# Performance work log

Hardware: AMD Instinct MI355X
Metric: run time of the kernel (lower is better)

The kernel has to match this reference:

```python
import jax, jax.numpy as jnp
import numpy as np

B, IN, O, F, FH = 512, 2000, 64, 8, 32
D = 64 + FH * O  # 2112


def setup_inputs() -> dict:
    key = jax.random.key(0)
    ks = jax.random.split(key, 17)
    rn = lambda k, s: jax.random.normal(k, s, dtype=jnp.float32) * 0.05
    return dict(
        x=rn(ks[0], (B, IN)),
        fc_in_W=rn(ks[1], (1024, IN)), fc_in_b=rn(ks[2], (1024,)),
        fc1_W=rn(ks[3], (128, 1024)), fc1_b=rn(ks[4], (128,)),
        out1_W=rn(ks[5], (O, 64, 128)), out1_b=rn(ks[6], (O, 64)),
        coef_nn_W=rn(ks[7], (F, FH, 1)), coef_nn_b=rn(ks[8], (F, FH)),
        coef_att_W=rn(ks[9], (F, FH, FH)),
        out_att_W=rn(ks[10], (O, FH, FH)),
        nodes_trans_W=rn(ks[11], (O, O)),
        trans_gcn_W=rn(ks[12], (D, D)),
        outmap_W=rn(ks[13], (1, D)), outmap_b=rn(ks[14], (1,)),
        prelu_a=jnp.float32(0.25),
        coef_m=rn(ks[15], (O, O, F)),
    )


def reference(x, fc_in_W, fc_in_b, fc1_W, fc1_b, out1_W, out1_b,
              coef_nn_W, coef_nn_b, coef_att_W, out_att_W,
              nodes_trans_W, trans_gcn_W, outmap_W, outmap_b, prelu_a, coef_m):
    elu = jax.nn.elu
    # trunk MLP
    h = jax.nn.relu(x @ fc_in_W.T + fc_in_b)          # [B,1024]
    h = jax.nn.relu(h @ fc1_W.T + fc1_b)              # [B,128]
    # per-output-node heads (vectorized over the output_dim loop)
    hiddens = jax.nn.relu(jnp.einsum('bk,odk->bod', h, out1_W) + out1_b)  # [B,O,64]
    # per-feature coef embedding: Linear(1,FH) on each coef_m[:,:,i] slice
    cf = elu(coef_m[..., None] * coef_nn_W[:, :, 0] + coef_nn_b)          # [O,O,F,FH]
    # sum over concatenated feature axis (F*FH) of exp(elu(.))
    s = jnp.exp(elu(cf)).sum(axis=(2, 3))[:, :, None, None]               # [O,O,1,1]
    lin = jnp.einsum('xyfh,fgh->xyfg', cf, coef_att_W)                    # per-feature attention linear
    p = elu(jnp.exp(elu(cf)) * lin / s)
    cfs = elu(p.sum(axis=2) / F)                                          # [O,O,FH]
    # node-level attention (vectorized over the output_dim loop)
    coef_sum = jnp.exp(elu(cfs)).sum(axis=1)                              # [O,FH]
    p2 = jnp.exp(elu(cfs)) / coef_sum[:, None, :]                         # [O,O,FH]
    lin2 = jnp.einsum('oih,igh->oig', cfs, out_att_W)
    att = (p2 * lin2).reshape(O, O * FH)                                  # concat over i (i-major)
    hc = jnp.concatenate(
        [hiddens, jnp.broadcast_to(att[None], (x.shape[0], O, O * FH))], axis=2)  # [B,O,D]
    nt = jnp.einsum('bpd,op->bod', hc, nodes_trans_W)                     # node mixing Linear(O,O)
    trans = jax.nn.sigmoid(jnp.einsum('bod,ed->boe', nt, trans_gcn_W))    # [B,O,D]
    z = (trans @ outmap_W.T + outmap_b).squeeze(-1)                       # [B,O]
    return jnp.where(z >= 0, z, prelu_a * z)                              # PReLU
```

## Files before the change

### kernel.cpp

```cpp
#include <hip/hip_runtime.h>
#include <math.h>

typedef __attribute__((ext_vector_type(8))) short bf16x8;
typedef __attribute__((ext_vector_type(4))) float f32x4;

static __device__ __forceinline__ float fast_elu(float x) {
    return x > 0.0f ? x : __expf(x) - 1.0f;
}

static __device__ __forceinline__ unsigned short f2bf(float f) {
    unsigned int u = __float_as_uint(f);
    unsigned int r = (u + 0x7FFFu + ((u >> 16) & 1u)) >> 16;
    return (unsigned short)r;
}

#define CV0 1048576
#define CV1 3145728
#define CV2 3276800
#define CV3 3280896
#define CV4 3805184
#define CV5 8265728
#define CONV_BLOCKS 32288

static __device__ __forceinline__ void conv_phase(
    int bx,
    const float* __restrict__ x, const float* __restrict__ fcinW,
    const float* __restrict__ fc1W, const float* __restrict__ ntW,
    const float* __restrict__ out1W, const float* __restrict__ tgw,
    unsigned short* __restrict__ xb, unsigned short* __restrict__ fcinWb,
    unsigned short* __restrict__ fc1Wb, unsigned short* __restrict__ Wb,
    unsigned short* __restrict__ out1WbT,
    unsigned short* __restrict__ Gb, unsigned short* __restrict__ G2b)
{
    int idx = bx * 256 + threadIdx.x;
    if (idx < CV0) {
        int r = idx >> 11, k = idx & 2047;
        xb[idx] = (k < 2000) ? f2bf(x[(size_t)r * 2000 + k]) : (unsigned short)0;
    } else if (idx < CV1) {
        int i = idx - CV0;
        int r = i >> 11, k = i & 2047;
        fcinWb[i] = (k < 2000) ? f2bf(fcinW[(size_t)r * 2000 + k]) : (unsigned short)0;
    } else if (idx < CV2) {
        int i = idx - CV1;
        fc1Wb[i] = f2bf(fc1W[i]);
    } else if (idx < CV3) {
        int i = idx - CV2;
        Wb[i] = f2bf(ntW[i]);
    } else if (idx < CV4) {
        int i = idx - CV3;
        int n = i >> 7, k = i & 127, d = n >> 6, p = n & 63;
        out1WbT[i] = f2bf(out1W[(size_t)((p << 6) | d) * 128 + k]);
    } else if (idx < CV5) {
        int i = idx - CV4;
        int e = i / 2112, k = i - e * 2112;
        unsigned short v = f2bf(tgw[(size_t)e * 2112 + k]);
        if (k < 64) Gb[e * 64 + k] = v;
        else        G2b[(size_t)e * 2048 + (k - 64)] = v;
    }
}

static __device__ __forceinline__ void coef_phase(
    int bx, float* __restrict__ smemf,
    const float* __restrict__ coef_m, const float* __restrict__ cW,
    const float* __restrict__ cB, const float* __restrict__ attW,
    float* __restrict__ cfs)
{
    float* cf_s = smemf;
    float* part = smemf + 1024;
    const int t = threadIdx.x;
    const int wv = t >> 6, lane = t & 63;
    const int xy = bx * 4 + wv;
    float ls = 0.0f;
    #pragma unroll
    for (int i = 0; i < 4; ++i) {
        int idx = i * 64 + lane;
        int f = idx >> 5;
        float v = fast_elu(coef_m[xy * 8 + f] * cW[idx] + cB[idx]);
        cf_s[wv * 256 + idx] = v;
        ls += __expf(fast_elu(v));
    }
    #pragma unroll
    for (int m = 1; m < 64; m <<= 1) ls += __shfl_xor(ls, m, 64);
    __syncthreads();
    const float rs = __builtin_amdgcn_rcpf(ls);
    const int g = lane & 31, fg = lane >> 5;
    float acc = 0.0f;
    for (int f = fg * 4; f < fg * 4 + 4; ++f) {
        float lin = 0.0f;
        #pragma unroll
        for (int h = 0; h < 32; h += 4) {
            float4 Lv = *reinterpret_cast<const float4*>(&cf_s[wv * 256 + f * 32 + h]);
            float4 Wv = *reinterpret_cast<const float4*>(&attW[f * 1024 + g * 32 + h]);
            lin += Lv.x * Wv.x + Lv.y * Wv.y + Lv.z * Wv.z + Lv.w * Wv.w;
        }
        float e = __expf(fast_elu(cf_s[wv * 256 + f * 32 + g]));
        acc += fast_elu(e * lin * rs);
    }
    part[wv * 64 + lane] = acc;
    __syncthreads();
    if (lane < 32) {
        float tot = part[wv * 64 + lane] + part[wv * 64 + lane + 32];
        cfs[xy * 32 + lane] = fast_elu(tot * 0.125f);
    }
}

static __device__ __forceinline__ void att_phase(
    int o, int ic, float* __restrict__ smemf,
    const float* __restrict__ cfs, const float* __restrict__ oattW,
    float* __restrict__ att)
{
    float* L    = smemf;
    float* red  = smemf + 2048;
    float* csum = smemf + 2304;
    const int t = threadIdx.x;
    #pragma unroll
    for (int j = 0; j < 8; ++j) L[t + 256 * j] = cfs[o * 2048 + t + 256 * j];
    __syncthreads();
    {
        int h = t & 31, ig = t >> 5;
        float ps = 0.0f;
        for (int i = ig * 8; i < ig * 8 + 8; ++i) ps += __expf(fast_elu(L[i * 32 + h]));
        red[t] = ps;
        __syncthreads();
        if (t < 32) {
            float cs = 0.0f;
            #pragma unroll
            for (int j = 0; j < 8; ++j) cs += red[j * 32 + t];
            csum[t] = cs;
        }
        __syncthreads();
    }
    int idx = ic * 256 + t;
    int i = idx >> 5, g = idx & 31;
    float lin2 = 0.0f;
    #pragma unroll
    for (int h = 0; h < 32; h += 4) {
        float4 Lv = *reinterpret_cast<const float4*>(&L[i * 32 + h]);
        float4 Wv = *reinterpret_cast<const float4*>(&oattW[i * 1024 + g * 32 + h]);
        lin2 += Lv.x * Wv.x + Lv.y * Wv.y + Lv.z * Wv.z + Lv.w * Wv.w;
    }
    float p2 = __expf(fast_elu(L[idx])) * __builtin_amdgcn_rcpf(csum[g]);
    att[o * 2048 + idx] = p2 * lin2;
}

static __device__ __forceinline__ void natt_phase(
    int bx, float* __restrict__ smemf,
    const float* __restrict__ ntW, const float* __restrict__ att,
    unsigned short* __restrict__ nattb)
{
    float* ntW_s = smemf;
    float* att_s = smemf + 64 * 65;
    const int t = threadIdx.x;
    const int d0 = bx * 16;
    #pragma unroll
    for (int j = 0; j < 16; ++j) {
        int idx = t + 256 * j;
        ntW_s[(idx >> 6) * 65 + (idx & 63)] = ntW[idx];
    }
    #pragma unroll
    for (int j = 0; j < 4; ++j) {
        int idx = t + 256 * j;
        int p = idx >> 4, dd = idx & 15;
        att_s[p * 17 + dd] = att[p * 2048 + d0 + dd];
    }
    __syncthreads();
    const int dd = t & 15, ob = (t >> 4) * 4;
    float acc[4] = {0.0f, 0.0f, 0.0f, 0.0f};
    for (int p = 0; p < 64; ++p) {
        float av = att_s[p * 17 + dd];
        #pragma unroll
        for (int i = 0; i < 4; ++i) acc[i] += ntW_s[(ob + i) * 65 + p] * av;
    }
    #pragma unroll
    for (int i = 0; i < 4; ++i)
        nattb[(ob + i) * 2048 + d0 + dd] = f2bf(acc[i]);
}

static __device__ __forceinline__ void gemm_core(
    const unsigned short* __restrict__ A, int lda,
    const unsigned short* __restrict__ B, int ldb,
    float* __restrict__ C, unsigned short* __restrict__ Cb,
    int ldc, long strideCz, const float* __restrict__ bias,
    int mode, int kchunk, int bn, int bm, int bz,
    unsigned short* __restrict__ As, unsigned short* __restrict__ Bs)
{
    const int t = threadIdx.x;
    const int w = t >> 6, lane = t & 63, l16 = lane & 15, quad = lane >> 4;
    const int n0 = bn * 64, m0 = bm * 64;
    const int kb0 = bz * kchunk;
    const int r = t >> 2, koff = (t & 3) * 8;
    if (mode == 0) C += (size_t)bz * strideCz;

    const size_t arow = (size_t)(m0 + r) * lda + koff;
    const size_t brow = (size_t)(n0 + r) * ldb + koff;
    bf16x8 av = *reinterpret_cast<const bf16x8*>(&A[arow + kb0]);
    bf16x8 bv = *reinterpret_cast<const bf16x8*>(&B[brow + kb0]);

    f32x4 acc[4] = {};
    for (int kb = kb0; kb < kb0 + kchunk; kb += 32) {
        __syncthreads();
        *reinterpret_cast<bf16x8*>(&As[r * 40 + koff]) = av;
        *reinterpret_cast<bf16x8*>(&Bs[r * 40 + koff]) = bv;
        if (kb + 32 < kb0 + kchunk) {
            av = *reinterpret_cast<const bf16x8*>(&A[arow + kb + 32]);
            bv = *reinterpret_cast<const bf16x8*>(&B[brow + kb + 32]);
        }
        __syncthreads();
        bf16x8 af = *reinterpret_cast<const bf16x8*>(&As[(w * 16 + l16) * 40 + quad * 8]);
        #pragma unroll
        for (int nt = 0; nt < 4; ++nt) {
            bf16x8 bf = *reinterpret_cast<const bf16x8*>(&Bs[(nt * 16 + l16) * 40 + quad * 8]);
            acc[nt] = __builtin_amdgcn_mfma_f32_16x16x32_bf16(af, bf, acc[nt], 0, 0, 0);
        }
    }
    #pragma unroll
    for (int nt = 0; nt < 4; ++nt)
        #pragma unroll
        for (int i = 0; i < 4; ++i) {
            int m = m0 + w * 16 + quad * 4 + i;
            int n = n0 + nt * 16 + l16;
            if (mode == 0) {
                C[(size_t)m * ldc + n] = acc[nt][i];
            } else {
                int bidx = (((n & 63) << 6) | (n >> 6));
                float v = acc[nt][i] + bias[bidx];
                v = fmaxf(v, 0.0f);
                Cb[(size_t)m * ldc + n] = f2bf(v);
            }
        }
}

static __device__ __forceinline__ void gemm_fa_core(
    const float* __restrict__ Ap, int lda, long apstride, int nparts,
    const float* __restrict__ abias,
    const unsigned short* __restrict__ B, int ldb,
    float* __restrict__ C, unsigned short* __restrict__ Cb,
    int ldc, long strideCz, const float* __restrict__ bias,
    int mode, int kchunk, int bn, int bm, int bz,
    unsigned short* __restrict__ As, unsigned short* __restrict__ Bs)
{
    const int t = threadIdx.x;
    const int w = t >> 6, lane = t & 63, l16 = lane & 15, quad = lane >> 4;
    const int n0 = bn * 64, m0 = bm * 64;
    const int kb0 = bz * kchunk;
    const int r = t >> 2, koff = (t & 3) * 8;
    if (mode == 0) C += (size_t)bz * strideCz;

    f32x4 acc[4] = {};
    for (int kb = kb0; kb < kb0 + kchunk; kb += 32) {
        float a8[8];
        {
            const float* base = &Ap[(size_t)(m0 + r) * lda + kb + koff];
            float4 s0 = *reinterpret_cast<const float4*>(base);
            float4 s1 = *reinterpret_cast<const float4*>(base + 4);
            for (int j = 1; j < nparts; ++j) {
                const float* pj = base + (size_t)j * apstride;
                float4 p0 = *reinterpret_cast<const float4*>(pj);
                float4 p1 = *reinterpret_cast<const float4*>(pj + 4);
                s0.x += p0.x; s0.y += p0.y; s0.z += p0.z; s0.w += p0.w;
                s1.x += p1.x; s1.y += p1.y; s1.z += p1.z; s1.w += p1.w;
            }
            float4 b0 = *reinterpret_cast<const float4*>(&abias[kb + koff]);
            float4 b1 = *reinterpret_cast<const float4*>(&abias[kb + koff + 4]);
            a8[0] = fmaxf(s0.x + b0.x, 0.0f); a8[1] = fmaxf(s0.y + b0.y, 0.0f);
            a8[2] = fmaxf(s0.z + b0.z, 0.0f); a8[3] = fmaxf(s0.w + b0.w, 0.0f);
            a8[4] = fmaxf(s1.x + b1.x, 0.0f); a8[5] = fmaxf(s1.y + b1.y, 0.0f);
            a8[6] = fmaxf(s1.z + b1.z, 0.0f); a8[7] = fmaxf(s1.w + b1.w, 0.0f);
        }
        bf16x8 bv = *reinterpret_cast<const bf16x8*>(&B[(size_t)(n0 + r) * ldb + kb + koff]);
        __syncthreads();
        ushort4 lo, hi;
        lo.x = f2bf(a8[0]); lo.y = f2bf(a8[1]); lo.z = f2bf(a8[2]); lo.w = f2bf(a8[3]);
        hi.x = f2bf(a8[4]); hi.y = f2bf(a8[5]); hi.z = f2bf(a8[6]); hi.w = f2bf(a8[7]);
        *reinterpret_cast<ushort4*>(&As[r * 40 + koff]) = lo;
        *reinterpret_cast<ushort4*>(&As[r * 40 + koff + 4]) = hi;
        *reinterpret_cast<bf16x8*>(&Bs[r * 40 + koff]) = bv;
        __syncthreads();
        bf16x8 af = *reinterpret_cast<const bf16x8*>(&As[(w * 16 + l16) * 40 + quad * 8]);
        #pragma unroll
        for (int nt = 0; nt < 4; ++nt) {
            bf16x8 bf = *reinterpret_cast<const bf16x8*>(&Bs[(nt * 16 + l16) * 40 + quad * 8]);
            acc[nt] = __builtin_amdgcn_mfma_f32_16x16x32_bf16(af, bf, acc[nt], 0, 0, 0);
        }
    }
    #pragma unroll
    for (int nt = 0; nt < 4; ++nt)
        #pragma unroll
        for (int i = 0; i < 4; ++i) {
            int m = m0 + w * 16 + quad * 4 + i;
            int n = n0 + nt * 16 + l16;
            if (mode == 0) {
                C[(size_t)m * ldc + n] = acc[nt][i];
            } else {
                int bidx = (((n & 63) << 6) | (n >> 6));
                float v = acc[nt][i] + bias[bidx];
                v = fmaxf(v, 0.0f);
                Cb[(size_t)m * ldc + n] = f2bf(v);
            }
        }
}

static __device__ __forceinline__ void nt1f_phase(
    int b, unsigned short* __restrict__ smemu,
    const unsigned short* __restrict__ hbT, const unsigned short* __restrict__ Wb,
    unsigned short* __restrict__ nt1b)
{
    unsigned short* HtT   = smemu;
    unsigned short* nt1_s = smemu + 64 * 72;
    const int t = threadIdx.x;
    const int w = t >> 6, lane = t & 63, l16 = lane & 15, quad = lane >> 4;

    const unsigned short* src = hbT + (size_t)b * 4096;
    #pragma unroll
    for (int j = 0; j < 2; ++j) {
        int c = t + j * 256;
        *reinterpret_cast<bf16x8*>(&HtT[(c >> 3) * 72 + (c & 7) * 8]) =
            *reinterpret_cast<const bf16x8*>(&src[c * 8]);
    }
    __syncthreads();

    bf16x8 aW[2];
    #pragma unroll
    for (int h = 0; h < 2; ++h)
        aW[h] = *reinterpret_cast<const bf16x8*>(&Wb[(w * 16 + l16) * 64 + h * 32 + quad * 8]);
    #pragma unroll
    for (int dt = 0; dt < 4; ++dt) {
        f32x4 acc = {0.0f, 0.0f, 0.0f, 0.0f};
        #pragma unroll
        for (int h = 0; h < 2; ++h) {
            bf16x8 bf = *reinterpret_cast<const bf16x8*>(
                &HtT[(dt * 16 + l16) * 72 + h * 32 + quad * 8]);
            acc = __builtin_amdgcn_mfma_f32_16x16x32_bf16(aW[h], bf, acc, 0, 0, 0);
        }
        #pragma unroll
        for (int i = 0; i < 4; ++i)
            nt1_s[(w * 16 + quad * 4 + i) * 72 + dt * 16 + l16] = f2bf(acc[i]);
    }
    __syncthreads();
    #pragma unroll
    for (int j = 0; j < 2; ++j) {
        int c = t + j * 256;
        *reinterpret_cast<bf16x8*>(&nt1b[(size_t)b * 4096 + c * 8]) =
            *reinterpret_cast<const bf16x8*>(&nt1_s[(c >> 3) * 72 + (c & 7) * 8]);
    }
}

__global__ __launch_bounds__(256) void uber1(
    const float* x, const float* fcinW, const float* fc1W, const float* ntW,
    const float* out1W, const float* tgw,
    unsigned short* xb, unsigned short* fcinWb, unsigned short* fc1Wb,
    unsigned short* Wb, unsigned short* out1WbT,
    unsigned short* Gb, unsigned short* G2b,
    const float* coef_m, const float* cW, const float* cB, const float* attW,
    float* cfs)
{
    __shared__ __align__(16) float smemf[1280];
    int bx = blockIdx.x;
    if (bx < CONV_BLOCKS)
        conv_phase(bx, x, fcinW, fc1W, ntW, out1W, tgw,
                   xb, fcinWb, fc1Wb, Wb, out1WbT, Gb, G2b);
    else
        coef_phase(bx - CONV_BLOCKS, smemf, coef_m, cW, cB, attW, cfs);
}

__global__ __launch_bounds__(256) void uber2(
    const unsigned short* xb, const unsigned short* fcinWb, float* h1p,
    const float* cfs, const float* oattW, float* att)
{
    __shared__ __align__(16) float smemf[2592];
    int bx = blockIdx.x;
    if (bx < 512) {
        unsigned short* As = (unsigned short*)smemf;
        gemm_core(xb, 2048, fcinWb, 2048, h1p, nullptr, 1024, 524288L,
                  nullptr, 0, 512, bx & 15, (bx >> 4) & 7, bx >> 7, As, As + 2560);
    } else {
        int b2 = bx - 512;
        att_phase(b2 & 63, b2 >> 6, smemf, cfs, oattW, att);
    }
}

__global__ __launch_bounds__(256) void uber3(
    const float* h1p, const float* fc_in_b, const unsigned short* fc1Wb,
    float* h2p,
    const float* ntW, const float* att, unsigned short* nattb)
{
    __shared__ __align__(16) float smemf[5248];
    int bx = blockIdx.x;
    if (bx < 64) {
        unsigned short* As = (unsigned short*)smemf;
        gemm_fa_core(h1p, 1024, 524288L, 4, fc_in_b, fc1Wb, 1024,
                     h2p, nullptr, 128, 65536L, nullptr, 0, 256,
                     bx & 1, (bx >> 1) & 7, bx >> 4, As, As + 2560);
    } else {
        natt_phase(bx - 64, smemf, ntW, att, nattb);
    }
}

__global__ __launch_bounds__(256) void uber4(
    const float* h2p, const float* fc1_b, const unsigned short* out1WbT,
    unsigned short* hbT, const float* out1_b,
    const unsigned short* G2b, const unsigned short* nattb, float* cpT)
{
    __shared__ __align__(16) float smemf[2560];
    unsigned short* As = (unsigned short*)smemf;
    int bx = blockIdx.x;
    if (bx < 512) {
        gemm_fa_core(h2p, 128, 65536L, 4, fc1_b, out1WbT, 128,
                     nullptr, hbT, 4096, 0L, out1_b, 2, 128,
                     bx & 63, bx >> 6, 0, As, As + 2560);
    } else {
        int b2 = bx - 512;
        gemm_core(G2b, 2048, nattb, 2048, cpT, nullptr, 64, 135168L,
                  nullptr, 0, 256, 0, b2 % 33, b2 / 33, As, As + 2560);
    }
}

__global__ __launch_bounds__(256) void uber5(
    const unsigned short* hbT, const unsigned short* Wb, unsigned short* nt1b,
    const float* cpT, float* cmatT)
{
    __shared__ __align__(16) unsigned short smemu[2 * 64 * 72];
    int bx = blockIdx.x;
    if (bx < 512) {
        nt1f_phase(bx, smemu, hbT, Wb, nt1b);
    } else {
        int i = (bx - 512) * 256 + threadIdx.x;
        if (i < 135168) {
            float a = 0.0f;
            #pragma unroll
            for (int j = 0; j < 8; ++j) a += cpT[i + (long)j * 135168L];
            cmatT[i] = a;
        }
    }
}

__global__ __launch_bounds__(256) void final_eblk(
    const unsigned short* __restrict__ nt1b,
    const unsigned short* __restrict__ Gb,
    const float* __restrict__ cmatT,
    const float* __restrict__ outW,
    float* __restrict__ zpart)
{
    __shared__ __align__(16) unsigned short nls[2][64 * 72];
    __shared__ float zs[2][4][64];
    const int t = threadIdx.x;
    const int w = t >> 6, lane = t & 63, l16 = lane & 15, quad = lane >> 4;
    const int eb = blockIdx.x;
    const int b0 = blockIdx.y * 16;
    const int ew = eb * 64 + w * 16;

    bf16x8 ga[2];
    #pragma unroll
    for (int h = 0; h < 2; ++h)
        ga[h] = *reinterpret_cast<const bf16x8*>(
            &Gb[(size_t)(ew + l16) * 64 + h * 32 + quad * 8]);
    float cm[4][4];
    #pragma unroll
    for (int nt = 0; nt < 4; ++nt)
        #pragma unroll
        for (int i = 0; i < 4; ++i)
            cm[nt][i] = cmatT[(size_t)(ew + quad * 4 + i) * 64 + nt * 16 + l16];
    float wv[4];
    #pragma unroll
    for (int i = 0; i < 4; ++i) wv[i] = outW[ew + quad * 4 + i];

    const int c0 = t, c1 = t + 256;
    bf16x8 v0 = *reinterpret_cast<const bf16x8*>(&nt1b[(size_t)b0 * 4096 + c0 * 8]);
    bf16x8 v1 = *reinterpret_cast<const bf16x8*>(&nt1b[(size_t)b0 * 4096 + c1 * 8]);
    *reinterpret_cast<bf16x8*>(&nls[0][(c0 >> 3) * 72 + (c0 & 7) * 8]) = v0;
    *reinterpret_cast<bf16x8*>(&nls[0][(c1 >> 3) * 72 + (c1 & 7) * 8]) = v1;
    __syncthreads();

    int cur = 0;
    for (int bi = 0; bi < 16; ++bi) {
        if (bi < 15) {
            v0 = *reinterpret_cast<const bf16x8*>(
                &nt1b[(size_t)(b0 + bi + 1) * 4096 + c0 * 8]);
            v1 = *reinterpret_cast<const bf16x8*>(
                &nt1b[(size_t)(b0 + bi + 1) * 4096 + c1 * 8]);
        }
        if (bi > 0 && t < 64) {
            const float* z = &zs[(bi - 1) & 1][0][0];
            zpart[((size_t)eb * 512 + b0 + bi - 1) * 64 + t] =
                z[t] + z[64 + t] + z[128 + t] + z[192 + t];
        }
        float zo[4] = {0.0f, 0.0f, 0.0f, 0.0f};
        #pragma unroll
        for (int nt = 0; nt < 4; ++nt) {
            bf16x8 bf0 = *reinterpret_cast<const bf16x8*>(
                &nls[cur][(nt * 16 + l16) * 72 + quad * 8]);
            bf16x8 bf1 = *reinterpret_cast<const bf16x8*>(
                &nls[cur][(nt * 16 + l16) * 72 + 32 + quad * 8]);
            f32x4 acc = {cm[nt][0], cm[nt][1], cm[nt][2], cm[nt][3]};
            acc = __builtin_amdgcn_mfma_f32_16x16x32_bf16(ga[0], bf0, acc, 0, 0, 0);
            acc = __builtin_amdgcn_mfma_f32_16x16x32_bf16(ga[1], bf1, acc, 0, 0, 0);
            #pragma unroll
            for (int i = 0; i < 4; ++i)
                zo[nt] += __builtin_amdgcn_rcpf(1.0f + __expf(-acc[i])) * wv[i];
        }
        #pragma unroll
        for (int nt = 0; nt < 4; ++nt) {
            zo[nt] += __shfl_xor(zo[nt], 16, 64);
            zo[nt] += __shfl_xor(zo[nt], 32, 64);
        }
        if (quad == 0) {
            #pragma unroll
            for (int nt = 0; nt < 4; ++nt)
                zs[bi & 1][w][nt * 16 + l16] = zo[nt];
        }
        if (bi < 15) {
            *reinterpret_cast<bf16x8*>(&nls[1 - cur][(c0 >> 3) * 72 + (c0 & 7) * 8]) = v0;
            *reinterpret_cast<bf16x8*>(&nls[1 - cur][(c1 >> 3) * 72 + (c1 & 7) * 8]) = v1;
        }
        __syncthreads();
        cur ^= 1;
    }
    if (t < 64) {
        const float* z = &zs[1][0][0];
        zpart[((size_t)eb * 512 + b0 + 15) * 64 + t] =
            z[t] + z[64 + t] + z[128 + t] + z[192 + t];
    }
}

__global__ __launch_bounds__(256) void finish_kernel(
    const float* __restrict__ zpart, const float* __restrict__ outB,
    const float* __restrict__ preluA, float* __restrict__ out)
{
    int i = blockIdx.x * 256 + threadIdx.x;
    float z = 0.0f;
    for (int j = 0; j < 33; ++j) z += zpart[(size_t)j * 32768 + i];
    z += outB[0];
    float pa = preluA[0];
    out[i] = (z >= 0.0f) ? z : pa * z;
}

extern "C" void kernel_launch(void* const* d_in, const int* in_sizes, int n_in,
                              void* d_out, int out_size, void* d_ws, size_t ws_size,
                              hipStream_t stream)
{
    const float* x       = (const float*)d_in[0];
    const float* fc_in_W = (const float*)d_in[1];
    const float* fc_in_b = (const float*)d_in[2];
    const float* fc1_W   = (const float*)d_in[3];
    const float* fc1_b   = (const float*)d_in[4];
    const float* out1_W  = (const float*)d_in[5];
    const float* out1_b  = (const float*)d_in[6];
    const float* cW      = (const float*)d_in[7];
    const float* cB      = (const float*)d_in[8];
    const float* cattW   = (const float*)d_in[9];
    const float* oattW   = (const float*)d_in[10];
    const float* ntW     = (const float*)d_in[11];
    const float* tgw     = (const float*)d_in[12];
    const float* outW    = (const float*)d_in[13];
    const float* outB    = (const float*)d_in[14];
    const float* preluA  = (const float*)d_in[15];
    const float* coef_m  = (const float*)d_in[16];
    float* out = (float*)d_out;
    float* ws  = (float*)d_ws;

    unsigned short* xb      = (unsigned short*)(ws + 0);
    unsigned short* fcinWb  = (unsigned short*)(ws + 524288);
    float*          cpT     = ws + 0;
    float*          h1p     = ws + 1572864;
    unsigned short* nt1b    = (unsigned short*)(ws + 1572864);
    float*          zpart   = ws + 2621440;
    unsigned short* fc1Wb   = (unsigned short*)(ws + 3670016);
    float*          h2p     = ws + 3735552;
    unsigned short* out1WbT = (unsigned short*)(ws + 3997696);
    unsigned short* hbT     = (unsigned short*)(ws + 4259840);
    unsigned short* Wb      = (unsigned short*)(ws + 5308416);
    unsigned short* Gb      = (unsigned short*)(ws + 5310464);
    unsigned short* G2b     = (unsigned short*)(ws + 5378048);
    float*          att     = ws + 7540736;
    unsigned short* nattb   = (unsigned short*)(ws + 7671808);
    float*          cmatT   = ws + 7737344;
    float*          cfs     = ws + 7737344;

    uber1<<<CONV_BLOCKS + 1024, 256, 0, stream>>>(
        x, fc_in_W, fc1_W, ntW, out1_W, tgw,
        xb, fcinWb, fc1Wb, Wb, out1WbT, Gb, G2b,
        coef_m, cW, cB, cattW, cfs);
    uber2<<<1024, 256, 0, stream>>>(xb, fcinWb, h1p, cfs, oattW, att);
    uber3<<<192, 256, 0, stream>>>(h1p, fc_in_b, fc1Wb, h2p, ntW, att, nattb);
    uber4<<<776, 256, 0, stream>>>(h2p, fc1_b, out1WbT, hbT, out1_b,
                                   G2b, nattb, cpT);
    uber5<<<1040, 256, 0, stream>>>(hbT, Wb, nt1b, cpT, cmatT);
    final_eblk<<<dim3(33, 32), 256, 0, stream>>>(nt1b, Gb, cmatT, outW, zpart);
    finish_kernel<<<128, 256, 0, stream>>>(zpart, outB, preluA, out);
}
```

Measured before the change: 201.1 us.

## Vectorize fp32-to-bf16 conversion and fuse trans_gcn weight conversion into GEMM

The conversion phase now has each thread convert eight floats with float4 loads and write one 16-byte bf16 vector, instead of one scalar element per thread. This cuts the conversion grid from tens of thousands of blocks to about two thousand. The 2112x2048 slice of trans_gcn_W is no longer converted to a bf16 buffer (G2b). The uber4 GEMM instead reads it as fp32 and converts it on the fly while staging the A tile, which removes a round trip through global memory. The cost is that the GEMM now reads twice the bytes per A element and has extra conversion ALU work inside its loop.

```diff
diff --git a/kernel.cpp b/kernel.cpp
--- a/kernel.cpp
+++ b/kernel.cpp
@@ -14,13 +14,24 @@
     return (unsigned short)r;
 }
 
-#define CV0 1048576
-#define CV1 3145728
-#define CV2 3276800
-#define CV3 3280896
-#define CV4 3805184
-#define CV5 8265728
-#define CONV_BLOCKS 32288
+static __device__ __forceinline__ bf16x8 cvt8(const float* __restrict__ s) {
+    float4 a = *reinterpret_cast<const float4*>(s);
+    float4 b = *reinterpret_cast<const float4*>(s + 4);
+    bf16x8 r;
+    r[0] = (short)f2bf(a.x); r[1] = (short)f2bf(a.y);
+    r[2] = (short)f2bf(a.z); r[3] = (short)f2bf(a.w);
+    r[4] = (short)f2bf(b.x); r[5] = (short)f2bf(b.y);
+    r[6] = (short)f2bf(b.z); r[7] = (short)f2bf(b.w);
+    return r;
+}
+
+#define S0 131072
+#define S1 393216
+#define S2 409600
+#define S3 410112
+#define S4 475648
+#define S5 492544
+#define CONV_BLOCKS 1924
 
 static __device__ __forceinline__ void conv_phase(
     int bx,
@@ -29,33 +40,39 @@
     const float* __restrict__ out1W, const float* __restrict__ tgw,
     unsigned short* __restrict__ xb, unsigned short* __restrict__ fcinWb,
     unsigned short* __restrict__ fc1Wb, unsigned short* __restrict__ Wb,
-    unsigned short* __restrict__ out1WbT,
-    unsigned short* __restrict__ Gb, unsigned short* __restrict__ G2b)
-{
-    int idx = bx * 256 + threadIdx.x;
-    if (idx < CV0) {
-        int r = idx >> 11, k = idx & 2047;
-        xb[idx] = (k < 2000) ? f2bf(x[(size_t)r * 2000 + k]) : (unsigned short)0;
-    } else if (idx < CV1) {
-        int i = idx - CV0;
-        int r = i >> 11, k = i & 2047;
-        fcinWb[i] = (k < 2000) ? f2bf(fcinW[(size_t)r * 2000 + k]) : (unsigned short)0;
-    } else if (idx < CV2) {
-        int i = idx - CV1;
-        fc1Wb[i] = f2bf(fc1W[i]);
-    } else if (idx < CV3) {
-        int i = idx - CV2;
-        Wb[i] = f2bf(ntW[i]);
-    } else if (idx < CV4) {
-        int i = idx - CV3;
-        int n = i >> 7, k = i & 127, d = n >> 6, p = n & 63;
-        out1WbT[i] = f2bf(out1W[(size_t)((p << 6) | d) * 128 + k]);
-    } else if (idx < CV5) {
-        int i = idx - CV4;
-        int e = i / 2112, k = i - e * 2112;
-        unsigned short v = f2bf(tgw[(size_t)e * 2112 + k]);
-        if (k < 64) Gb[e * 64 + k] = v;
-        else        G2b[(size_t)e * 2048 + (k - 64)] = v;
+    unsigned short* __restrict__ out1WbT, unsigned short* __restrict__ Gb)
+{
+    int u = bx * 256 + threadIdx.x;
+    if (u < S0) {
+        int r = u >> 8, c = u & 255;
+        bf16x8 v;
+        if (c < 250) v = cvt8(&x[(size_t)r * 2000 + c * 8]);
+        else { bf16x8 z = {0,0,0,0,0,0,0,0}; v = z; }
+        *reinterpret_cast<bf16x8*>(&xb[(size_t)r * 2048 + c * 8]) = v;
+    } else if (u < S1) {
+        int i = u - S0;
+        int r = i >> 8, c = i & 255;
+        bf16x8 v;
+        if (c < 250) v = cvt8(&fcinW[(size_t)r * 2000 + c * 8]);
+        else { bf16x8 z = {0,0,0,0,0,0,0,0}; v = z; }
+        *reinterpret_cast<bf16x8*>(&fcinWb[(size_t)r * 2048 + c * 8]) = v;
+    } else if (u < S2) {
+        int i8 = (u - S1) * 8;
+        *reinterpret_cast<bf16x8*>(&fc1Wb[i8]) = cvt8(&fc1W[i8]);
+    } else if (u < S3) {
+        int i8 = (u - S2) * 8;
+        *reinterpret_cast<bf16x8*>(&Wb[i8]) = cvt8(&ntW[i8]);
+    } else if (u < S4) {
+        int i = u - S3;
+        int n = i >> 4, kc = i & 15;
+        int d = n >> 6, p = n & 63;
+        *reinterpret_cast<bf16x8*>(&out1WbT[(size_t)n * 128 + kc * 8]) =
+            cvt8(&out1W[(size_t)((p << 6) | d) * 128 + kc * 8]);
+    } else if (u < S5) {
+        int i = u - S4;
+        int e = i >> 3, c = i & 7;
+        *reinterpret_cast<bf16x8*>(&Gb[(size_t)e * 64 + c * 8]) =
+            cvt8(&tgw[(size_t)e * 2112 + c * 8]);
     }
 }
 
@@ -227,6 +244,52 @@
                 v = fmaxf(v, 0.0f);
                 Cb[(size_t)m * ldc + n] = f2bf(v);
             }
+        }
+}
+
+static __device__ __forceinline__ void gemm_tgwa_core(
+    const float* __restrict__ tgw,
+    const unsigned short* __restrict__ B,
+    float* __restrict__ C, long strideCz,
+    int kchunk, int bm, int bz,
+    unsigned short* __restrict__ As, unsigned short* __restrict__ Bs)
+{
+    const int t = threadIdx.x;
+    const int w = t >> 6, lane = t & 63, l16 = lane & 15, quad = lane >> 4;
+    const int m0 = bm * 64;
+    const int kb0 = bz * kchunk;
+    const int r = t >> 2, koff = (t & 3) * 8;
+    C += (size_t)bz * strideCz;
+
+    const float* arow = tgw + (size_t)(m0 + r) * 2112 + 64 + koff;
+    const unsigned short* brow = B + (size_t)r * 2048 + koff;
+    bf16x8 av = cvt8(arow + kb0);
+    bf16x8 bv = *reinterpret_cast<const bf16x8*>(brow + kb0);
+
+    f32x4 acc[4] = {};
+    for (int kb = kb0; kb < kb0 + kchunk; kb += 32) {
+        __syncthreads();
+        *reinterpret_cast<bf16x8*>(&As[r * 40 + koff]) = av;
+        *reinterpret_cast<bf16x8*>(&Bs[r * 40 + koff]) = bv;
+        if (kb + 32 < kb0 + kchunk) {
+            av = cvt8(arow + kb + 32);
+            bv = *reinterpret_cast<const bf16x8*>(brow + kb + 32);
+        }
+        __syncthreads();
+        bf16x8 af = *reinterpret_cast<const bf16x8*>(&As[(w * 16 + l16) * 40 + quad * 8]);
+        #pragma unroll
+        for (int nt = 0; nt < 4; ++nt) {
+            bf16x8 bf = *reinterpret_cast<const bf16x8*>(&Bs[(nt * 16 + l16) * 40 + quad * 8]);
+            acc[nt] = __builtin_amdgcn_mfma_f32_16x16x32_bf16(af, bf, acc[nt], 0, 0, 0);
+        }
+    }
+    #pragma unroll
+    for (int nt = 0; nt < 4; ++nt)
+        #pragma unroll
+        for (int i = 0; i < 4; ++i) {
+            int m = m0 + w * 16 + quad * 4 + i;
+            int n = nt * 16 + l16;
+            C[(size_t)m * 64 + n] = acc[nt][i];
         }
 }
 
@@ -349,8 +412,7 @@
     const float* x, const float* fcinW, const float* fc1W, const float* ntW,
     const float* out1W, const float* tgw,
     unsigned short* xb, unsigned short* fcinWb, unsigned short* fc1Wb,
-    unsigned short* Wb, unsigned short* out1WbT,
-    unsigned short* Gb, unsigned short* G2b,
+    unsigned short* Wb, unsigned short* out1WbT, unsigned short* Gb,
     const float* coef_m, const float* cW, const float* cB, const float* attW,
     float* cfs)
 {
@@ -358,7 +420,7 @@
     int bx = blockIdx.x;
     if (bx < CONV_BLOCKS)
         conv_phase(bx, x, fcinW, fc1W, ntW, out1W, tgw,
-                   xb, fcinWb, fc1Wb, Wb, out1WbT, Gb, G2b);
+                   xb, fcinWb, fc1Wb, Wb, out1WbT, Gb);
     else
         coef_phase(bx - CONV_BLOCKS, smemf, coef_m, cW, cB, attW, cfs);
 }
@@ -399,7 +461,7 @@
 __global__ __launch_bounds__(256) void uber4(
     const float* h2p, const float* fc1_b, const unsigned short* out1WbT,
     unsigned short* hbT, const float* out1_b,
-    const unsigned short* G2b, const unsigned short* nattb, float* cpT)
+    const float* tgw, const unsigned short* nattb, float* cpT)
 {
     __shared__ __align__(16) float smemf[2560];
     unsigned short* As = (unsigned short*)smemf;
@@ -410,8 +472,8 @@
                      bx & 63, bx >> 6, 0, As, As + 2560);
     } else {
         int b2 = bx - 512;
-        gemm_core(G2b, 2048, nattb, 2048, cpT, nullptr, 64, 135168L,
-                  nullptr, 0, 256, 0, b2 % 33, b2 / 33, As, As + 2560);
+        gemm_tgwa_core(tgw, nattb, cpT, 135168L, 256,
+                       b2 % 33, b2 / 33, As, As + 2560);
     }
 }
 
@@ -570,7 +632,6 @@
     unsigned short* hbT     = (unsigned short*)(ws + 4259840);
     unsigned short* Wb      = (unsigned short*)(ws + 5308416);
     unsigned short* Gb      = (unsigned short*)(ws + 5310464);
-    unsigned short* G2b     = (unsigned short*)(ws + 5378048);
     float*          att     = ws + 7540736;
     unsigned short* nattb   = (unsigned short*)(ws + 7671808);
     float*          cmatT   = ws + 7737344;
@@ -578,12 +639,12 @@
 
     uber1<<<CONV_BLOCKS + 1024, 256, 0, stream>>>(
         x, fc_in_W, fc1_W, ntW, out1_W, tgw,
-        xb, fcinWb, fc1Wb, Wb, out1WbT, Gb, G2b,
+        xb, fcinWb, fc1Wb, Wb, out1WbT, Gb,
         coef_m, cW, cB, cattW, cfs);
     uber2<<<1024, 256, 0, stream>>>(xb, fcinWb, h1p, cfs, oattW, att);
     uber3<<<192, 256, 0, stream>>>(h1p, fc_in_b, fc1Wb, h2p, ntW, att, nattb);
     uber4<<<776, 256, 0, stream>>>(h2p, fc1_b, out1WbT, hbT, out1_b,
-                                   G2b, nattb, cpT);
+                                   tgw, nattb, cpT);
     uber5<<<1040, 256, 0, stream>>>(hbT, Wb, nt1b, cpT, cmatT);
     final_eblk<<<dim3(33, 32), 256, 0, stream>>>(nt1b, Gb, cmatT, outW, zpart);
     finish_kernel<<<128, 256, 0, stream>>>(zpart, outB, preluA, out);
```

New measurement: 194.9 us. -3.1%, faster.
